# Kernel optimization log

Hardware: AMD Instinct MI355X
Metric: run time of the kernel (lower is better)

The kernel has to match this reference:

```python
import jax, jax.numpy as jnp
import numpy as np

WIN = (7, 7)
SHIFT = (3, 3)
HEADS = 8


def _rel_index():
    coords = np.stack(np.meshgrid(np.arange(WIN[0]), np.arange(WIN[1]), indexing='ij')).reshape(2, -1)
    rel = (coords[:, :, None] - coords[:, None, :]).transpose(1, 2, 0)  # [N,N,2]
    rel[:, :, 0] += WIN[0] - 1
    rel[:, :, 1] += WIN[1] - 1
    rel[:, :, 0] *= 2 * WIN[1] - 1
    return jnp.asarray(rel.sum(-1).reshape(-1).astype(np.int32))  # [N*N]


def _attn_mask(pad_H, pad_W):
    # standard Swin shifted-window mask (intended behavior of the source's mask block)
    img = np.zeros((pad_H, pad_W), np.float32)
    cnt = 0
    for h in ((0, -WIN[0]), (-WIN[0], -SHIFT[0]), (-SHIFT[0], None)):
        for w in ((0, -WIN[1]), (-WIN[1], -SHIFT[1]), (-SHIFT[1], None)):
            img[h[0]:h[1], w[0]:w[1]] = cnt
            cnt += 1
    nHw, nWw = pad_H // WIN[0], pad_W // WIN[1]
    m = img.reshape(nHw, WIN[0], nWw, WIN[1]).transpose(0, 2, 1, 3).reshape(nHw * nWw, WIN[0] * WIN[1])
    diff = m[:, None, :] - m[:, :, None]  # [nW, N, N]
    return jnp.asarray(np.where(diff != 0, -100.0, 0.0).astype(np.float32))


def setup_inputs() -> dict:
    key = jax.random.key(0)
    ks = jax.random.split(key, 6)
    B, H, W, C = 32, 56, 56, 256
    return {
        'x': jax.random.normal(ks[0], (B, H, W, C), jnp.float32),
        'qkv_weight': jax.random.normal(ks[1], (3 * C, C), jnp.float32) * (C ** -0.5),
        'qkv_bias': jnp.zeros((3 * C,), jnp.float32),
        'proj_weight': jax.random.normal(ks[2], (C, C), jnp.float32) * (C ** -0.5),
        'proj_bias': jnp.zeros((C,), jnp.float32),
        'rel_bias_table': jax.random.normal(ks[3], ((2 * WIN[0] - 1) * (2 * WIN[1] - 1), HEADS), jnp.float32) * 0.02,
        'rel_index': _rel_index(),
    }


def reference(x, qkv_weight, qkv_bias, proj_weight, proj_bias, rel_bias_table, rel_index):
    B, H, W, C = x.shape
    hd = C // HEADS
    N = WIN[0] * WIN[1]
    # relative position bias: [1, heads, N, N]
    bias = rel_bias_table[rel_index].reshape(N, N, HEADS).transpose(2, 0, 1)[None]
    # H, W chosen divisible by window -> pad is a no-op; cyclic shift
    xs = jnp.roll(x, (-SHIFT[0], -SHIFT[1]), axis=(1, 2))
    nHw, nWw = H // WIN[0], W // WIN[1]
    nW = nHw * nWw
    xw = xs.reshape(B, nHw, WIN[0], nWw, WIN[1], C).transpose(0, 1, 3, 2, 4, 5).reshape(B * nW, N, C)
    qkv = xw @ qkv_weight.T + qkv_bias                           # [B*nW, N, 3C]
    qkv = qkv.reshape(B * nW, N, 3, HEADS, hd).transpose(2, 0, 3, 1, 4)
    q, k, v = qkv[0] * hd ** -0.5, qkv[1], qkv[2]                # [B*nW, heads, N, hd]
    attn = jnp.einsum('whnd,whmd->whnm', q, k) + bias            # [B*nW, heads, N, N]
    mask = _attn_mask(H, W)                                      # [nW, N, N]
    attn = attn.reshape(B, nW, HEADS, N, N) + mask[None, :, None]
    attn = jax.nn.softmax(attn, axis=-1).reshape(B * nW, HEADS, N, N)
    out = jnp.einsum('whnm,whmd->wnhd', attn, v).reshape(B * nW, N, C)
    out = out @ proj_weight.T + proj_bias
    out = out.reshape(B, nHw, nWw, WIN[0], WIN[1], C).transpose(0, 1, 3, 2, 4, 5).reshape(B, H, W, C)
    out = jnp.roll(out, (SHIFT[0], SHIFT[1]), axis=(1, 2))
    return out
```

## Files before the change

kernel.cpp:

```cpp
#include <hip/hip_runtime.h>

typedef float f32x4 __attribute__((ext_vector_type(4)));
typedef __bf16 bf16x4 __attribute__((ext_vector_type(4)));
typedef __bf16 bf16x8 __attribute__((ext_vector_type(8)));
typedef short s16x4 __attribute__((ext_vector_type(4)));

#define DEVI static __device__ __forceinline__

DEVI f32x4 mfma_k32(bf16x8 a, bf16x8 b, f32x4 c) {
    return __builtin_amdgcn_mfma_f32_16x16x32_bf16(a, b, c, 0, 0, 0);
}

union B4 { bf16x4 h; s16x4 s; };
DEVI f32x4 mfma_k16(bf16x4 a, bf16x4 b, f32x4 c) {
    B4 ua, ub; ua.h = a; ub.h = b;
    return __builtin_amdgcn_mfma_f32_16x16x16bf16_1k(ua.s, ub.s, c, 0, 0, 0);
}

union F8 { bf16x8 v; bf16x4 h[2]; };

DEVI bf16x8 ld8_lds(const __bf16* p) {
    F8 f;
    f.h[0] = *(const bf16x4*)p;
    f.h[1] = *(const bf16x4*)(p + 4);
    return f.v;
}
DEVI bf16x8 ld8_gb(const __bf16* p) { return *(const bf16x8*)p; }
DEVI bf16x8 ldf8(const float* p) {
    f32x4 a = *(const f32x4*)p;
    f32x4 b = *(const f32x4*)(p + 4);
    F8 f;
#pragma unroll
    for (int j = 0; j < 4; ++j) {
        f.h[0][j] = (__bf16)a[j];
        f.h[1][j] = (__bf16)b[j];
    }
    return f.v;
}
DEVI bf16x4 pk4(f32x4 v) {
    bf16x4 r;
#pragma unroll
    for (int j = 0; j < 4; ++j) r[j] = (__bf16)v[j];
    return r;
}

__global__ __launch_bounds__(256) void k_pre(const float* __restrict__ wqkv,
                                             const float* __restrict__ wp,
                                             const float* __restrict__ btab,
                                             __bf16* __restrict__ wout,
                                             float* __restrict__ bmout) {
    int bid = blockIdx.x;
    if (bid < 128) {
        int i = bid * 256 + threadIdx.x;
        int t = i >> 9, kc = (i >> 6) & 7, l = i & 63;
        int row = t * 16 + (l & 15);
        int col = kc * 32 + (l >> 4) * 8;
        const float* src = (t < 48) ? (wqkv + row * 256 + col)
                                    : (wp + (row - 768) * 256 + col);
        f32x4 a = *(const f32x4*)src;
        f32x4 b = *(const f32x4*)(src + 4);
        F8 f;
#pragma unroll
        for (int j = 0; j < 4; ++j) { f.h[0][j] = (__bf16)a[j]; f.h[1][j] = (__bf16)b[j]; }
        *(bf16x8*)(wout + (size_t)i * 8) = f.v;
    } else {
        int i = (bid - 128) * 256 + threadIdx.x;
        int r = i & 3, lane = (i >> 2) & 63;
        int kt = (i >> 8) & 3, qt = (i >> 10) & 3, h = (i >> 12) & 7, cls = i >> 15;
        int li = lane & 15, g = lane >> 4;
        int q = 16 * qt + li;
        int key = 16 * kt + 4 * g + r;
        float v;
        if (key >= 49) {
            v = -30000.f;
        } else if (q >= 49) {
            v = 0.f;
        } else {
            int qi = q / 7, qj = q - 7 * qi;
            int ki = key / 7, kj = key - 7 * ki;
            float bias = btab[((qi - ki + 6) * 13 + (qj - kj + 6)) * 8 + h];
            int ch = cls >> 1, cw = cls & 1;
            int gq = (ch ? (qi < 4 ? 1 : 2) : 0) * 3 + (cw ? (qj < 4 ? 1 : 2) : 0);
            int gk = (ch ? (ki < 4 ? 1 : 2) : 0) * 3 + (cw ? (kj < 4 ? 1 : 2) : 0);
            v = bias + ((gq != gk) ? -100.f : 0.f);
        }
        bmout[i] = v;
    }
}

__global__ __launch_bounds__(512)
__attribute__((amdgpu_waves_per_eu(4))) void k_swin(
    const float* __restrict__ x,
    const __bf16* __restrict__ wb,
    const float* __restrict__ bqkv,
    const float* __restrict__ bm,
    const float* __restrict__ pbias,
    float* __restrict__ out)
{
    __shared__ __align__(16) unsigned char smem[51216];
    __bf16* xw = (__bf16*)(smem);
    __bf16* cb = (__bf16*)(smem + 25480);
    unsigned* obase = (unsigned*)(smem + 50960);

    const int tid = threadIdx.x;
    const int wid = tid >> 6, lane = tid & 63;
    const int li = lane & 15, g = lane >> 4;
    const int blk = blockIdx.x;
    const int b = blk >> 6, wi = blk & 63;
    const int wh = wi >> 3, ww = wi & 7;
    const int h = wid;
    const int cls = ((wh == 7) ? 2 : 0) + ((ww == 7) ? 1 : 0);

    for (int c = tid; c < 49 * 32; c += 512) {
        int tok = c >> 5, part = c & 31;
        int i = tok / 7, j = tok - 7 * i;
        int r = wh * 7 + i + 3;  if (r >= 56) r -= 56;
        int cc = ww * 7 + j + 3; if (cc >= 56) cc -= 56;
        F8 f; f.v = ldf8(x + (((size_t)(b * 56 + r) * 56 + cc) << 8) + (part << 3));
        __bf16* dst = xw + tok * 260 + (part << 3);
        *(bf16x4*)dst = f.h[0];
        *(bf16x4*)(dst + 4) = f.h[1];
    }
    if (tid < 49) {
        int i = tid / 7, j = tid - 7 * i;
        int r = wh * 7 + i + 3;  if (r >= 56) r -= 56;
        int cc = ww * 7 + j + 3; if (cc >= 56) cc -= 56;
        obase[tid] = ((unsigned)((b * 56 + r) * 56 + cc)) << 8;
    }
    __syncthreads();

    const f32x4 zf = {0.f, 0.f, 0.f, 0.f};
    const __bf16* wqb = wb + (size_t)(2 * h) * 4096 + lane * 8;
    const __bf16* wkb = wqb + 16 * 4096;
    const __bf16* wvb = wqb + 32 * 4096;

    bf16x4 qf[4][2], kf[4][2];
    {
        f32x4 qa[2][4], ka[2][4];
#pragma unroll
        for (int ct = 0; ct < 2; ++ct)
#pragma unroll
            for (int tt = 0; tt < 4; ++tt) { qa[ct][tt] = zf; ka[ct][tt] = zf; }

#pragma unroll
        for (int kc = 0; kc < 8; ++kc) {
            bf16x8 xf[4];
#pragma unroll
            for (int tt = 0; tt < 4; ++tt) {
                int row = 16 * tt + li; if (row > 48) row = 48;
                xf[tt] = ld8_lds(xw + row * 260 + kc * 32 + g * 8);
            }
#pragma unroll
            for (int ct = 0; ct < 2; ++ct) {
                bf16x8 aq = ld8_gb(wqb + ct * 4096 + kc * 512);
                bf16x8 ak = ld8_gb(wkb + ct * 4096 + kc * 512);
#pragma unroll
                for (int tt = 0; tt < 4; ++tt) {
                    qa[ct][tt] = mfma_k32(aq, xf[tt], qa[ct][tt]);
                    ka[ct][tt] = mfma_k32(ak, xf[tt], ka[ct][tt]);
                }
            }
        }
#pragma unroll
        for (int ct = 0; ct < 2; ++ct) {
            f32x4 bq = *(const f32x4*)(bqkv + h * 32 + 16 * ct + 4 * g);
            f32x4 bk = *(const f32x4*)(bqkv + 256 + h * 32 + 16 * ct + 4 * g);
#pragma unroll
            for (int tt = 0; tt < 4; ++tt)
#pragma unroll
                for (int r = 0; r < 4; ++r) {
                    qf[tt][ct][r] = (__bf16)((qa[ct][tt][r] + bq[r]) * 0.17677669529663687f);
                    kf[tt][ct][r] = (__bf16)(ka[ct][tt][r] + bk[r]);
                }
        }
    }
    __builtin_amdgcn_sched_barrier(0);

    bf16x4 vf[2][4];
    {
        f32x4 va[4][2];
#pragma unroll
        for (int tt = 0; tt < 4; ++tt)
#pragma unroll
            for (int ct = 0; ct < 2; ++ct) va[tt][ct] = zf;
#pragma unroll
        for (int kc = 0; kc < 8; ++kc) {
            bf16x8 bv0 = ld8_gb(wvb + kc * 512);
            bf16x8 bv1 = ld8_gb(wvb + 4096 + kc * 512);
#pragma unroll
            for (int tt = 0; tt < 4; ++tt) {
                int row = 16 * tt + li; if (row > 48) row = 48;
                bf16x8 xf = ld8_lds(xw + row * 260 + kc * 32 + g * 8);
                va[tt][0] = mfma_k32(xf, bv0, va[tt][0]);
                va[tt][1] = mfma_k32(xf, bv1, va[tt][1]);
            }
        }
#pragma unroll
        for (int ct = 0; ct < 2; ++ct) {
            float bv = bqkv[512 + h * 32 + 16 * ct + li];
#pragma unroll
            for (int tt = 0; tt < 4; ++tt)
#pragma unroll
                for (int r = 0; r < 4; ++r)
                    vf[ct][tt][r] = (__bf16)(va[tt][ct][r] + bv);
        }
    }
    __builtin_amdgcn_sched_barrier(0);

    const float* bmq = bm + cls * 32768 + h * 4096 + lane * 4;
    bf16x4 osv[4][2];
#pragma unroll
    for (int qt = 0; qt < 4; ++qt) {
        f32x4 sv[4];
#pragma unroll
        for (int kt = 0; kt < 4; ++kt) {
            f32x4 acc = *(const f32x4*)(bmq + qt * 1024 + kt * 256);
            acc = mfma_k16(kf[kt][0], qf[qt][0], acc);
            acc = mfma_k16(kf[kt][1], qf[qt][1], acc);
            sv[kt] = acc;
        }
        float mx = fmaxf(fmaxf(sv[0][0], sv[0][1]), fmaxf(sv[0][2], sv[0][3]));
#pragma unroll
        for (int kt = 1; kt < 4; ++kt)
#pragma unroll
            for (int r = 0; r < 4; ++r) mx = fmaxf(mx, sv[kt][r]);
        mx = fmaxf(mx, __shfl_xor(mx, 16));
        mx = fmaxf(mx, __shfl_xor(mx, 32));
        float sum = 0.f;
#pragma unroll
        for (int kt = 0; kt < 4; ++kt)
#pragma unroll
            for (int r = 0; r < 4; ++r) {
                float e = __expf(sv[kt][r] - mx);
                sv[kt][r] = e;
                sum += e;
            }
        sum += __shfl_xor(sum, 16);
        sum += __shfl_xor(sum, 32);
        float inv = 1.0f / sum;
        bf16x4 pp[4];
#pragma unroll
        for (int kt = 0; kt < 4; ++kt)
#pragma unroll
            for (int r = 0; r < 4; ++r) pp[kt][r] = (__bf16)(sv[kt][r] * inv);
#pragma unroll
        for (int dt = 0; dt < 2; ++dt) {
            f32x4 acc = zf;
#pragma unroll
            for (int kt = 0; kt < 4; ++kt)
                acc = mfma_k16(pp[kt], vf[dt][kt], acc);
            osv[qt][dt] = pk4(acc);
        }
    }

#pragma unroll
    for (int qt = 0; qt < 4; ++qt)
#pragma unroll
        for (int r = 0; r < 4; ++r) {
            int q = 16 * qt + 4 * g + r;
            if (q < 49) {
#pragma unroll
                for (int dt = 0; dt < 2; ++dt)
                    cb[q * 260 + 32 * h + 16 * dt + li] = osv[qt][dt][r];
            }
        }
    __syncthreads();

    const int pm = wid >> 2, pn = wid & 3;
    f32x4 pacc[2][4];
#pragma unroll
    for (int mt = 0; mt < 2; ++mt)
#pragma unroll
        for (int nt = 0; nt < 4; ++nt) pacc[mt][nt] = zf;

    const __bf16* wpb = wb + (size_t)(48 + 4 * pn) * 4096 + lane * 8;
#pragma unroll
    for (int kc = 0; kc < 8; ++kc) {
        bf16x8 a[2];
#pragma unroll
        for (int mt = 0; mt < 2; ++mt) {
            int row = 32 * pm + 16 * mt + li; if (row > 48) row = 48;
            a[mt] = ld8_lds(cb + row * 260 + kc * 32 + g * 8);
        }
#pragma unroll
        for (int nt = 0; nt < 4; ++nt) {
            bf16x8 bb = ld8_gb(wpb + nt * 4096 + kc * 512);
#pragma unroll
            for (int mt = 0; mt < 2; ++mt)
                pacc[mt][nt] = mfma_k32(a[mt], bb, pacc[mt][nt]);
        }
    }

#pragma unroll
    for (int nt = 0; nt < 4; ++nt) {
        int o = 64 * pn + 16 * nt + li;
        float bias = pbias[o];
#pragma unroll
        for (int mt = 0; mt < 2; ++mt)
#pragma unroll
            for (int r = 0; r < 4; ++r) {
                int n = 32 * pm + 16 * mt + 4 * g + r;
                if (n < 49)
                    out[obase[n] + (unsigned)o] = pacc[mt][nt][r] + bias;
            }
    }
}

extern "C" void kernel_launch(void* const* d_in, const int* in_sizes, int n_in,
                              void* d_out, int out_size, void* d_ws, size_t ws_size,
                              hipStream_t stream) {
    const float* x    = (const float*)d_in[0];
    const float* wqkv = (const float*)d_in[1];
    const float* bqkv = (const float*)d_in[2];
    const float* wp   = (const float*)d_in[3];
    const float* pb   = (const float*)d_in[4];
    const float* btab = (const float*)d_in[5];
    float* out = (float*)d_out;

    __bf16* wbuf = (__bf16*)d_ws;
    float* bm = (float*)((char*)d_ws + 524288);
    k_pre<<<640, 256, 0, stream>>>(wqkv, wp, btab, wbuf, bm);
    k_swin<<<2048, 512, 0, stream>>>(x, wbuf, bqkv, bm, pb, out);
}
```

Measured before the change: 275.7 us.

## Process four windows per block with double-buffered x staging and prefetch

Each block now handles four consecutive windows instead of one, and the grid shrinks from 2048 to 512 blocks. The x tile is double-buffered in LDS: the next window's fp32 input is loaded into registers during the attention phase and written as bf16 after it, so global load latency overlaps compute. The softmax also drops its row-max subtraction and adds the bias/mask after the MFMA rather than using it as the accumulator init. The trade-offs are more LDS per block (lower occupancy), a grid of exactly one wave, and exposure to exp overflow if logits are ever large.

```diff
diff --git a/kernel.cpp b/kernel.cpp
--- a/kernel.cpp
+++ b/kernel.cpp
@@ -26,22 +26,31 @@
     return f.v;
 }
 DEVI bf16x8 ld8_gb(const __bf16* p) { return *(const bf16x8*)p; }
-DEVI bf16x8 ldf8(const float* p) {
-    f32x4 a = *(const f32x4*)p;
-    f32x4 b = *(const f32x4*)(p + 4);
-    F8 f;
-#pragma unroll
-    for (int j = 0; j < 4; ++j) {
-        f.h[0][j] = (__bf16)a[j];
-        f.h[1][j] = (__bf16)b[j];
-    }
-    return f.v;
-}
 DEVI bf16x4 pk4(f32x4 v) {
     bf16x4 r;
 #pragma unroll
     for (int j = 0; j < 4; ++j) r[j] = (__bf16)v[j];
     return r;
+}
+
+DEVI size_t stage_src_off(int w, int t) {
+    int bb = w >> 6, wi = w & 63, wh = wi >> 3, ww = wi & 7;
+    int tok = t >> 3, p0 = (t & 7) * 4;
+    int i = tok / 7, j = tok - 7 * i;
+    int r = wh * 7 + i + 3;  if (r >= 56) r -= 56;
+    int cc = ww * 7 + j + 3; if (cc >= 56) cc -= 56;
+    return (((size_t)(bb * 56 + r) * 56 + cc) << 8) + (p0 << 3);
+}
+DEVI int stage_dst_off(int t) {
+    int tok = t >> 3, p0 = (t & 7) * 4;
+    return tok * 260 + p0 * 8;
+}
+DEVI unsigned out_base(int w, int tok) {
+    int bb = w >> 6, wi = w & 63, wh = wi >> 3, ww = wi & 7;
+    int i = tok / 7, j = tok - 7 * i;
+    int r = wh * 7 + i + 3;  if (r >= 56) r -= 56;
+    int cc = ww * 7 + j + 3; if (cc >= 56) cc -= 56;
+    return ((unsigned)((bb * 56 + r) * 56 + cc)) << 8;
 }
 
 __global__ __launch_bounds__(256) void k_pre(const float* __restrict__ wqkv,
@@ -97,212 +106,237 @@
     const float* __restrict__ pbias,
     float* __restrict__ out)
 {
-    __shared__ __align__(16) unsigned char smem[51216];
-    __bf16* xw = (__bf16*)(smem);
-    __bf16* cb = (__bf16*)(smem + 25480);
-    unsigned* obase = (unsigned*)(smem + 50960);
+    __shared__ __align__(16) unsigned char smem[76840];
+    __bf16* xw0 = (__bf16*)(smem);
+    __bf16* cb = (__bf16*)(smem + 50960);
+    unsigned* obase = (unsigned*)(smem + 76440);
 
     const int tid = threadIdx.x;
     const int wid = tid >> 6, lane = tid & 63;
     const int li = lane & 15, g = lane >> 4;
-    const int blk = blockIdx.x;
-    const int b = blk >> 6, wi = blk & 63;
-    const int wh = wi >> 3, ww = wi & 7;
     const int h = wid;
-    const int cls = ((wh == 7) ? 2 : 0) + ((ww == 7) ? 1 : 0);
-
-    for (int c = tid; c < 49 * 32; c += 512) {
-        int tok = c >> 5, part = c & 31;
-        int i = tok / 7, j = tok - 7 * i;
-        int r = wh * 7 + i + 3;  if (r >= 56) r -= 56;
-        int cc = ww * 7 + j + 3; if (cc >= 56) cc -= 56;
-        F8 f; f.v = ldf8(x + (((size_t)(b * 56 + r) * 56 + cc) << 8) + (part << 3));
-        __bf16* dst = xw + tok * 260 + (part << 3);
-        *(bf16x4*)dst = f.h[0];
-        *(bf16x4*)(dst + 4) = f.h[1];
-    }
-    if (tid < 49) {
-        int i = tid / 7, j = tid - 7 * i;
-        int r = wh * 7 + i + 3;  if (r >= 56) r -= 56;
-        int cc = ww * 7 + j + 3; if (cc >= 56) cc -= 56;
-        obase[tid] = ((unsigned)((b * 56 + r) * 56 + cc)) << 8;
-    }
-    __syncthreads();
-
+    const int pm = wid >> 2, pn = wid & 3;
     const f32x4 zf = {0.f, 0.f, 0.f, 0.f};
+
     const __bf16* wqb = wb + (size_t)(2 * h) * 4096 + lane * 8;
     const __bf16* wkb = wqb + 16 * 4096;
     const __bf16* wvb = wqb + 32 * 4096;
-
-    bf16x4 qf[4][2], kf[4][2];
-    {
-        f32x4 qa[2][4], ka[2][4];
-#pragma unroll
-        for (int ct = 0; ct < 2; ++ct)
-#pragma unroll
-            for (int tt = 0; tt < 4; ++tt) { qa[ct][tt] = zf; ka[ct][tt] = zf; }
+    const __bf16* wpb = wb + (size_t)(48 + 4 * pn) * 4096 + lane * 8;
+
+    const int w0 = blockIdx.x * 4;
+
+    if (tid < 392) {
+        f32x4 sa[4][2];
+        const float* p = x + stage_src_off(w0, tid);
+#pragma unroll
+        for (int s = 0; s < 4; ++s) {
+            sa[s][0] = *(const f32x4*)(p + s * 8);
+            sa[s][1] = *(const f32x4*)(p + s * 8 + 4);
+        }
+        __bf16* dst = xw0 + stage_dst_off(tid);
+#pragma unroll
+        for (int s = 0; s < 4; ++s) {
+            F8 f;
+#pragma unroll
+            for (int j = 0; j < 4; ++j) {
+                f.h[0][j] = (__bf16)sa[s][0][j];
+                f.h[1][j] = (__bf16)sa[s][1][j];
+            }
+            *(bf16x4*)(dst + s * 8) = f.h[0];
+            *(bf16x4*)(dst + s * 8 + 4) = f.h[1];
+        }
+    }
+    if (tid < 49) obase[tid] = out_base(w0, tid);
+    __syncthreads();
+
+    for (int it = 0; it < 4; ++it) {
+        const int w = w0 + it;
+        const int wi = w & 63;
+        const int cls = (((wi >> 3) == 7) ? 2 : 0) + (((wi & 7) == 7) ? 1 : 0);
+        const int cur = it & 1, nxt = cur ^ 1;
+        const __bf16* xwc = xw0 + cur * 12740;
+
+        bf16x4 qf[4][2], kf[4][2];
+        {
+            f32x4 qa[2][4], ka[2][4];
+#pragma unroll
+            for (int ct = 0; ct < 2; ++ct)
+#pragma unroll
+                for (int tt = 0; tt < 4; ++tt) { qa[ct][tt] = zf; ka[ct][tt] = zf; }
+
+#pragma unroll
+            for (int kc = 0; kc < 8; ++kc) {
+                bf16x8 xf[4];
+#pragma unroll
+                for (int tt = 0; tt < 4; ++tt) {
+                    int row = 16 * tt + li; if (row > 48) row = 48;
+                    xf[tt] = ld8_lds(xwc + row * 260 + kc * 32 + g * 8);
+                }
+#pragma unroll
+                for (int ct = 0; ct < 2; ++ct) {
+                    bf16x8 aq = ld8_gb(wqb + ct * 4096 + kc * 512);
+                    bf16x8 ak = ld8_gb(wkb + ct * 4096 + kc * 512);
+#pragma unroll
+                    for (int tt = 0; tt < 4; ++tt) {
+                        qa[ct][tt] = mfma_k32(aq, xf[tt], qa[ct][tt]);
+                        ka[ct][tt] = mfma_k32(ak, xf[tt], ka[ct][tt]);
+                    }
+                }
+            }
+#pragma unroll
+            for (int ct = 0; ct < 2; ++ct) {
+                f32x4 bq = *(const f32x4*)(bqkv + h * 32 + 16 * ct + 4 * g);
+                f32x4 bk = *(const f32x4*)(bqkv + 256 + h * 32 + 16 * ct + 4 * g);
+#pragma unroll
+                for (int tt = 0; tt < 4; ++tt)
+#pragma unroll
+                    for (int r = 0; r < 4; ++r) {
+                        qf[tt][ct][r] = (__bf16)((qa[ct][tt][r] + bq[r]) * 0.17677669529663687f);
+                        kf[tt][ct][r] = (__bf16)(ka[ct][tt][r] + bk[r]);
+                    }
+            }
+        }
+        __builtin_amdgcn_sched_barrier(0);
+
+        bf16x4 vf[2][4];
+        {
+            f32x4 va[4][2];
+#pragma unroll
+            for (int tt = 0; tt < 4; ++tt)
+#pragma unroll
+                for (int ct = 0; ct < 2; ++ct) va[tt][ct] = zf;
+#pragma unroll
+            for (int kc = 0; kc < 8; ++kc) {
+                bf16x8 bv0 = ld8_gb(wvb + kc * 512);
+                bf16x8 bv1 = ld8_gb(wvb + 4096 + kc * 512);
+#pragma unroll
+                for (int tt = 0; tt < 4; ++tt) {
+                    int row = 16 * tt + li; if (row > 48) row = 48;
+                    bf16x8 xf = ld8_lds(xwc + row * 260 + kc * 32 + g * 8);
+                    va[tt][0] = mfma_k32(xf, bv0, va[tt][0]);
+                    va[tt][1] = mfma_k32(xf, bv1, va[tt][1]);
+                }
+            }
+#pragma unroll
+            for (int ct = 0; ct < 2; ++ct) {
+                float bv = bqkv[512 + h * 32 + 16 * ct + li];
+#pragma unroll
+                for (int tt = 0; tt < 4; ++tt)
+#pragma unroll
+                    for (int r = 0; r < 4; ++r)
+                        vf[ct][tt][r] = (__bf16)(va[tt][ct][r] + bv);
+            }
+        }
+        __builtin_amdgcn_sched_barrier(0);
+
+        const bool hn = (it < 3);
+        f32x4 sa[4][2];
+        if (hn && tid < 392) {
+            const float* p = x + stage_src_off(w + 1, tid);
+#pragma unroll
+            for (int s = 0; s < 4; ++s) {
+                sa[s][0] = *(const f32x4*)(p + s * 8);
+                sa[s][1] = *(const f32x4*)(p + s * 8 + 4);
+            }
+        }
+
+        const float* bmq = bm + cls * 32768 + h * 4096 + lane * 4;
+#pragma unroll
+        for (int qt = 0; qt < 4; ++qt) {
+            f32x4 sv[4];
+#pragma unroll
+            for (int kt = 0; kt < 4; ++kt) {
+                f32x4 acc = zf;
+                acc = mfma_k16(kf[kt][0], qf[qt][0], acc);
+                acc = mfma_k16(kf[kt][1], qf[qt][1], acc);
+                sv[kt] = acc + *(const f32x4*)(bmq + qt * 1024 + kt * 256);
+            }
+            float sum = 0.f;
+#pragma unroll
+            for (int kt = 0; kt < 4; ++kt)
+#pragma unroll
+                for (int r = 0; r < 4; ++r) {
+                    float e = __expf(sv[kt][r]);
+                    sv[kt][r] = e;
+                    sum += e;
+                }
+            sum += __shfl_xor(sum, 16);
+            sum += __shfl_xor(sum, 32);
+            float inv = 1.0f / sum;
+            bf16x4 pp[4];
+#pragma unroll
+            for (int kt = 0; kt < 4; ++kt)
+#pragma unroll
+                for (int r = 0; r < 4; ++r) pp[kt][r] = (__bf16)(sv[kt][r] * inv);
+#pragma unroll
+            for (int dt = 0; dt < 2; ++dt) {
+                f32x4 acc = zf;
+#pragma unroll
+                for (int kt = 0; kt < 4; ++kt)
+                    acc = mfma_k16(pp[kt], vf[dt][kt], acc);
+                bf16x4 o4 = pk4(acc);
+#pragma unroll
+                for (int r = 0; r < 4; ++r) {
+                    int q = 16 * qt + 4 * g + r;
+                    if (q < 49) cb[q * 260 + 32 * h + 16 * dt + li] = o4[r];
+                }
+            }
+        }
+
+        if (hn && tid < 392) {
+            __bf16* dst = xw0 + nxt * 12740 + stage_dst_off(tid);
+#pragma unroll
+            for (int s = 0; s < 4; ++s) {
+                F8 f;
+#pragma unroll
+                for (int j = 0; j < 4; ++j) {
+                    f.h[0][j] = (__bf16)sa[s][0][j];
+                    f.h[1][j] = (__bf16)sa[s][1][j];
+                }
+                *(bf16x4*)(dst + s * 8) = f.h[0];
+                *(bf16x4*)(dst + s * 8 + 4) = f.h[1];
+            }
+        }
+        if (hn && tid < 49) obase[nxt * 49 + tid] = out_base(w + 1, tid);
+        __syncthreads();
+
+        f32x4 pacc[2][4];
+#pragma unroll
+        for (int mt = 0; mt < 2; ++mt)
+#pragma unroll
+            for (int nt = 0; nt < 4; ++nt) pacc[mt][nt] = zf;
 
 #pragma unroll
         for (int kc = 0; kc < 8; ++kc) {
-            bf16x8 xf[4];
-#pragma unroll
-            for (int tt = 0; tt < 4; ++tt) {
-                int row = 16 * tt + li; if (row > 48) row = 48;
-                xf[tt] = ld8_lds(xw + row * 260 + kc * 32 + g * 8);
-            }
-#pragma unroll
-            for (int ct = 0; ct < 2; ++ct) {
-                bf16x8 aq = ld8_gb(wqb + ct * 4096 + kc * 512);
-                bf16x8 ak = ld8_gb(wkb + ct * 4096 + kc * 512);
-#pragma unroll
-                for (int tt = 0; tt < 4; ++tt) {
-                    qa[ct][tt] = mfma_k32(aq, xf[tt], qa[ct][tt]);
-                    ka[ct][tt] = mfma_k32(ak, xf[tt], ka[ct][tt]);
-                }
-            }
-        }
-#pragma unroll
-        for (int ct = 0; ct < 2; ++ct) {
-            f32x4 bq = *(const f32x4*)(bqkv + h * 32 + 16 * ct + 4 * g);
-            f32x4 bk = *(const f32x4*)(bqkv + 256 + h * 32 + 16 * ct + 4 * g);
-#pragma unroll
-            for (int tt = 0; tt < 4; ++tt)
+            bf16x8 a[2];
+#pragma unroll
+            for (int mt = 0; mt < 2; ++mt) {
+                int row = 32 * pm + 16 * mt + li; if (row > 48) row = 48;
+                a[mt] = ld8_lds(cb + row * 260 + kc * 32 + g * 8);
+            }
+#pragma unroll
+            for (int nt = 0; nt < 4; ++nt) {
+                bf16x8 bb = ld8_gb(wpb + nt * 4096 + kc * 512);
+#pragma unroll
+                for (int mt = 0; mt < 2; ++mt)
+                    pacc[mt][nt] = mfma_k32(a[mt], bb, pacc[mt][nt]);
+            }
+        }
+
+#pragma unroll
+        for (int nt = 0; nt < 4; ++nt) {
+            int o = 64 * pn + 16 * nt + li;
+            float bias = pbias[o];
+#pragma unroll
+            for (int mt = 0; mt < 2; ++mt)
 #pragma unroll
                 for (int r = 0; r < 4; ++r) {
-                    qf[tt][ct][r] = (__bf16)((qa[ct][tt][r] + bq[r]) * 0.17677669529663687f);
-                    kf[tt][ct][r] = (__bf16)(ka[ct][tt][r] + bk[r]);
-                }
-        }
-    }
-    __builtin_amdgcn_sched_barrier(0);
-
-    bf16x4 vf[2][4];
-    {
-        f32x4 va[4][2];
-#pragma unroll
-        for (int tt = 0; tt < 4; ++tt)
-#pragma unroll
-            for (int ct = 0; ct < 2; ++ct) va[tt][ct] = zf;
-#pragma unroll
-        for (int kc = 0; kc < 8; ++kc) {
-            bf16x8 bv0 = ld8_gb(wvb + kc * 512);
-            bf16x8 bv1 = ld8_gb(wvb + 4096 + kc * 512);
-#pragma unroll
-            for (int tt = 0; tt < 4; ++tt) {
-                int row = 16 * tt + li; if (row > 48) row = 48;
-                bf16x8 xf = ld8_lds(xw + row * 260 + kc * 32 + g * 8);
-                va[tt][0] = mfma_k32(xf, bv0, va[tt][0]);
-                va[tt][1] = mfma_k32(xf, bv1, va[tt][1]);
-            }
-        }
-#pragma unroll
-        for (int ct = 0; ct < 2; ++ct) {
-            float bv = bqkv[512 + h * 32 + 16 * ct + li];
-#pragma unroll
-            for (int tt = 0; tt < 4; ++tt)
-#pragma unroll
-                for (int r = 0; r < 4; ++r)
-                    vf[ct][tt][r] = (__bf16)(va[tt][ct][r] + bv);
-        }
-    }
-    __builtin_amdgcn_sched_barrier(0);
-
-    const float* bmq = bm + cls * 32768 + h * 4096 + lane * 4;
-    bf16x4 osv[4][2];
-#pragma unroll
-    for (int qt = 0; qt < 4; ++qt) {
-        f32x4 sv[4];
-#pragma unroll
-        for (int kt = 0; kt < 4; ++kt) {
-            f32x4 acc = *(const f32x4*)(bmq + qt * 1024 + kt * 256);
-            acc = mfma_k16(kf[kt][0], qf[qt][0], acc);
-            acc = mfma_k16(kf[kt][1], qf[qt][1], acc);
-            sv[kt] = acc;
-        }
-        float mx = fmaxf(fmaxf(sv[0][0], sv[0][1]), fmaxf(sv[0][2], sv[0][3]));
-#pragma unroll
-        for (int kt = 1; kt < 4; ++kt)
-#pragma unroll
-            for (int r = 0; r < 4; ++r) mx = fmaxf(mx, sv[kt][r]);
-        mx = fmaxf(mx, __shfl_xor(mx, 16));
-        mx = fmaxf(mx, __shfl_xor(mx, 32));
-        float sum = 0.f;
-#pragma unroll
-        for (int kt = 0; kt < 4; ++kt)
-#pragma unroll
-            for (int r = 0; r < 4; ++r) {
-                float e = __expf(sv[kt][r] - mx);
-                sv[kt][r] = e;
-                sum += e;
-            }
-        sum += __shfl_xor(sum, 16);
-        sum += __shfl_xor(sum, 32);
-        float inv = 1.0f / sum;
-        bf16x4 pp[4];
-#pragma unroll
-        for (int kt = 0; kt < 4; ++kt)
-#pragma unroll
-            for (int r = 0; r < 4; ++r) pp[kt][r] = (__bf16)(sv[kt][r] * inv);
-#pragma unroll
-        for (int dt = 0; dt < 2; ++dt) {
-            f32x4 acc = zf;
-#pragma unroll
-            for (int kt = 0; kt < 4; ++kt)
-                acc = mfma_k16(pp[kt], vf[dt][kt], acc);
-            osv[qt][dt] = pk4(acc);
-        }
-    }
-
-#pragma unroll
-    for (int qt = 0; qt < 4; ++qt)
-#pragma unroll
-        for (int r = 0; r < 4; ++r) {
-            int q = 16 * qt + 4 * g + r;
-            if (q < 49) {
-#pragma unroll
-                for (int dt = 0; dt < 2; ++dt)
-                    cb[q * 260 + 32 * h + 16 * dt + li] = osv[qt][dt][r];
-            }
-        }
-    __syncthreads();
-
-    const int pm = wid >> 2, pn = wid & 3;
-    f32x4 pacc[2][4];
-#pragma unroll
-    for (int mt = 0; mt < 2; ++mt)
-#pragma unroll
-        for (int nt = 0; nt < 4; ++nt) pacc[mt][nt] = zf;
-
-    const __bf16* wpb = wb + (size_t)(48 + 4 * pn) * 4096 + lane * 8;
-#pragma unroll
-    for (int kc = 0; kc < 8; ++kc) {
-        bf16x8 a[2];
-#pragma unroll
-        for (int mt = 0; mt < 2; ++mt) {
-            int row = 32 * pm + 16 * mt + li; if (row > 48) row = 48;
-            a[mt] = ld8_lds(cb + row * 260 + kc * 32 + g * 8);
-        }
-#pragma unroll
-        for (int nt = 0; nt < 4; ++nt) {
-            bf16x8 bb = ld8_gb(wpb + nt * 4096 + kc * 512);
-#pragma unroll
-            for (int mt = 0; mt < 2; ++mt)
-                pacc[mt][nt] = mfma_k32(a[mt], bb, pacc[mt][nt]);
-        }
-    }
-
-#pragma unroll
-    for (int nt = 0; nt < 4; ++nt) {
-        int o = 64 * pn + 16 * nt + li;
-        float bias = pbias[o];
-#pragma unroll
-        for (int mt = 0; mt < 2; ++mt)
-#pragma unroll
-            for (int r = 0; r < 4; ++r) {
-                int n = 32 * pm + 16 * mt + 4 * g + r;
-                if (n < 49)
-                    out[obase[n] + (unsigned)o] = pacc[mt][nt][r] + bias;
-            }
+                    int n = 32 * pm + 16 * mt + 4 * g + r;
+                    if (n < 49)
+                        out[obase[cur * 49 + n] + (unsigned)o] = pacc[mt][nt][r] + bias;
+                }
+        }
+        __syncthreads();
     }
 }
 
@@ -320,5 +354,5 @@
     __bf16* wbuf = (__bf16*)d_ws;
     float* bm = (float*)((char*)d_ws + 524288);
     k_pre<<<640, 256, 0, stream>>>(wqkv, wp, btab, wbuf, bm);
-    k_swin<<<2048, 512, 0, stream>>>(x, wbuf, bqkv, bm, pb, out);
-}
+    k_swin<<<512, 512, 0, stream>>>(x, wbuf, bqkv, bm, pb, out);
+}
```

Measured after the change: 691.6 us. +150.8%, slower.

## Fold softmax scaling into weights, drop max pass, vectorize attention and output stores

Applied to the files above, without the earlier changes.

The Q scale and log2(e) are folded into the packed Q weights, and log2(e) into the bias/mask table. The per-row max reduction is removed, and the softmax now uses a hardware exp2 and rcp, with normalization applied after the PV product. QKV and projection biases now initialise the MFMA accumulators instead of being added afterwards. The PV and projection MFMA operands are swapped so each lane holds contiguous channels, which gives bf16x4 LDS stores and f32x4 global output stores in place of scalar ones. Skipping the max subtraction risks overflow if the logits become large.

```diff
diff --git a/kernel.cpp b/kernel.cpp
--- a/kernel.cpp
+++ b/kernel.cpp
@@ -7,6 +7,9 @@
 
 #define DEVI static __device__ __forceinline__
 
+#define LOG2E 1.4426950408889634f
+#define QSCALE (0.17677669529663687f * 1.4426950408889634f)
+
 DEVI f32x4 mfma_k32(bf16x8 a, bf16x8 b, f32x4 c) {
     return __builtin_amdgcn_mfma_f32_16x16x32_bf16(a, b, c, 0, 0, 0);
 }
@@ -16,6 +19,9 @@
     B4 ua, ub; ua.h = a; ub.h = b;
     return __builtin_amdgcn_mfma_f32_16x16x16bf16_1k(ua.s, ub.s, c, 0, 0, 0);
 }
+
+DEVI float exp2_hw(float x) { return __builtin_amdgcn_exp2f(x); }
+DEVI float rcp_hw(float x)  { return __builtin_amdgcn_rcpf(x); }
 
 union F8 { bf16x8 v; bf16x4 h[2]; };
 
@@ -57,11 +63,15 @@
         int col = kc * 32 + (l >> 4) * 8;
         const float* src = (t < 48) ? (wqkv + row * 256 + col)
                                     : (wp + (row - 768) * 256 + col);
+        float s = (t < 16) ? QSCALE : 1.0f;
         f32x4 a = *(const f32x4*)src;
         f32x4 b = *(const f32x4*)(src + 4);
         F8 f;
 #pragma unroll
-        for (int j = 0; j < 4; ++j) { f.h[0][j] = (__bf16)a[j]; f.h[1][j] = (__bf16)b[j]; }
+        for (int j = 0; j < 4; ++j) {
+            f.h[0][j] = (__bf16)(a[j] * s);
+            f.h[1][j] = (__bf16)(b[j] * s);
+        }
         *(bf16x8*)(wout + (size_t)i * 8) = f.v;
     } else {
         int i = (bid - 128) * 256 + threadIdx.x;
@@ -84,7 +94,7 @@
             int gk = (ch ? (ki < 4 ? 1 : 2) : 0) * 3 + (cw ? (kj < 4 ? 1 : 2) : 0);
             v = bias + ((gq != gk) ? -100.f : 0.f);
         }
-        bmout[i] = v;
+        bmout[i] = v * LOG2E;
     }
 }
 
@@ -136,11 +146,17 @@
 
     bf16x4 qf[4][2], kf[4][2];
     {
+        f32x4 bq[2], bk[2];
+#pragma unroll
+        for (int ct = 0; ct < 2; ++ct) {
+            bq[ct] = *(const f32x4*)(bqkv + h * 32 + 16 * ct + 4 * g) * QSCALE;
+            bk[ct] = *(const f32x4*)(bqkv + 256 + h * 32 + 16 * ct + 4 * g);
+        }
         f32x4 qa[2][4], ka[2][4];
 #pragma unroll
         for (int ct = 0; ct < 2; ++ct)
 #pragma unroll
-            for (int tt = 0; tt < 4; ++tt) { qa[ct][tt] = zf; ka[ct][tt] = zf; }
+            for (int tt = 0; tt < 4; ++tt) { qa[ct][tt] = bq[ct]; ka[ct][tt] = bk[ct]; }
 
 #pragma unroll
         for (int kc = 0; kc < 8; ++kc) {
@@ -162,53 +178,50 @@
             }
         }
 #pragma unroll
-        for (int ct = 0; ct < 2; ++ct) {
-            f32x4 bq = *(const f32x4*)(bqkv + h * 32 + 16 * ct + 4 * g);
-            f32x4 bk = *(const f32x4*)(bqkv + 256 + h * 32 + 16 * ct + 4 * g);
+        for (int ct = 0; ct < 2; ++ct)
 #pragma unroll
             for (int tt = 0; tt < 4; ++tt)
 #pragma unroll
                 for (int r = 0; r < 4; ++r) {
-                    qf[tt][ct][r] = (__bf16)((qa[ct][tt][r] + bq[r]) * 0.17677669529663687f);
-                    kf[tt][ct][r] = (__bf16)(ka[ct][tt][r] + bk[r]);
+                    qf[tt][ct][r] = (__bf16)qa[ct][tt][r];
+                    kf[tt][ct][r] = (__bf16)ka[ct][tt][r];
                 }
-        }
     }
     __builtin_amdgcn_sched_barrier(0);
 
     bf16x4 vf[2][4];
     {
+        float bv0 = bqkv[512 + h * 32 + li];
+        float bv1 = bqkv[512 + h * 32 + 16 + li];
         f32x4 va[4][2];
 #pragma unroll
-        for (int tt = 0; tt < 4; ++tt)
-#pragma unroll
-            for (int ct = 0; ct < 2; ++ct) va[tt][ct] = zf;
+        for (int tt = 0; tt < 4; ++tt) {
+            va[tt][0] = (f32x4){bv0, bv0, bv0, bv0};
+            va[tt][1] = (f32x4){bv1, bv1, bv1, bv1};
+        }
 #pragma unroll
         for (int kc = 0; kc < 8; ++kc) {
-            bf16x8 bv0 = ld8_gb(wvb + kc * 512);
-            bf16x8 bv1 = ld8_gb(wvb + 4096 + kc * 512);
+            bf16x8 bvw0 = ld8_gb(wvb + kc * 512);
+            bf16x8 bvw1 = ld8_gb(wvb + 4096 + kc * 512);
 #pragma unroll
             for (int tt = 0; tt < 4; ++tt) {
                 int row = 16 * tt + li; if (row > 48) row = 48;
                 bf16x8 xf = ld8_lds(xw + row * 260 + kc * 32 + g * 8);
-                va[tt][0] = mfma_k32(xf, bv0, va[tt][0]);
-                va[tt][1] = mfma_k32(xf, bv1, va[tt][1]);
+                va[tt][0] = mfma_k32(xf, bvw0, va[tt][0]);
+                va[tt][1] = mfma_k32(xf, bvw1, va[tt][1]);
             }
         }
 #pragma unroll
-        for (int ct = 0; ct < 2; ++ct) {
-            float bv = bqkv[512 + h * 32 + 16 * ct + li];
+        for (int ct = 0; ct < 2; ++ct)
 #pragma unroll
             for (int tt = 0; tt < 4; ++tt)
 #pragma unroll
                 for (int r = 0; r < 4; ++r)
-                    vf[ct][tt][r] = (__bf16)(va[tt][ct][r] + bv);
-        }
+                    vf[ct][tt][r] = (__bf16)va[tt][ct][r];
     }
     __builtin_amdgcn_sched_barrier(0);
 
     const float* bmq = bm + cls * 32768 + h * 4096 + lane * 4;
-    bf16x4 osv[4][2];
 #pragma unroll
     for (int qt = 0; qt < 4; ++qt) {
         f32x4 sv[4];
@@ -219,61 +232,51 @@
             acc = mfma_k16(kf[kt][1], qf[qt][1], acc);
             sv[kt] = acc;
         }
-        float mx = fmaxf(fmaxf(sv[0][0], sv[0][1]), fmaxf(sv[0][2], sv[0][3]));
-#pragma unroll
-        for (int kt = 1; kt < 4; ++kt)
-#pragma unroll
-            for (int r = 0; r < 4; ++r) mx = fmaxf(mx, sv[kt][r]);
-        mx = fmaxf(mx, __shfl_xor(mx, 16));
-        mx = fmaxf(mx, __shfl_xor(mx, 32));
         float sum = 0.f;
 #pragma unroll
         for (int kt = 0; kt < 4; ++kt)
 #pragma unroll
             for (int r = 0; r < 4; ++r) {
-                float e = __expf(sv[kt][r] - mx);
+                float e = exp2_hw(sv[kt][r]);
                 sv[kt][r] = e;
                 sum += e;
             }
         sum += __shfl_xor(sum, 16);
         sum += __shfl_xor(sum, 32);
-        float inv = 1.0f / sum;
+        float inv = rcp_hw(sum);
         bf16x4 pp[4];
 #pragma unroll
         for (int kt = 0; kt < 4; ++kt)
 #pragma unroll
-            for (int r = 0; r < 4; ++r) pp[kt][r] = (__bf16)(sv[kt][r] * inv);
+            for (int r = 0; r < 4; ++r) pp[kt][r] = (__bf16)sv[kt][r];
+        const int q = 16 * qt + li;
 #pragma unroll
         for (int dt = 0; dt < 2; ++dt) {
             f32x4 acc = zf;
 #pragma unroll
             for (int kt = 0; kt < 4; ++kt)
-                acc = mfma_k16(pp[kt], vf[dt][kt], acc);
-            osv[qt][dt] = pk4(acc);
-        }
-    }
-
-#pragma unroll
-    for (int qt = 0; qt < 4; ++qt)
-#pragma unroll
-        for (int r = 0; r < 4; ++r) {
-            int q = 16 * qt + 4 * g + r;
-            if (q < 49) {
-#pragma unroll
-                for (int dt = 0; dt < 2; ++dt)
-                    cb[q * 260 + 32 * h + 16 * dt + li] = osv[qt][dt][r];
-            }
-        }
+                acc = mfma_k16(vf[dt][kt], pp[kt], acc);
+            acc *= inv;
+            bf16x4 o4 = pk4(acc);
+            if (q < 49)
+                *(bf16x4*)(cb + q * 260 + 32 * h + 16 * dt + 4 * g) = o4;
+        }
+    }
     __syncthreads();
 
     const int pm = wid >> 2, pn = wid & 3;
+    const __bf16* wpb = wb + (size_t)(48 + 4 * pn) * 4096 + lane * 8;
+
+    f32x4 pb4[4];
+#pragma unroll
+    for (int nt = 0; nt < 4; ++nt)
+        pb4[nt] = *(const f32x4*)(pbias + 64 * pn + 16 * nt + 4 * g);
     f32x4 pacc[2][4];
 #pragma unroll
     for (int mt = 0; mt < 2; ++mt)
 #pragma unroll
-        for (int nt = 0; nt < 4; ++nt) pacc[mt][nt] = zf;
-
-    const __bf16* wpb = wb + (size_t)(48 + 4 * pn) * 4096 + lane * 8;
+        for (int nt = 0; nt < 4; ++nt) pacc[mt][nt] = pb4[nt];
+
 #pragma unroll
     for (int kc = 0; kc < 8; ++kc) {
         bf16x8 a[2];
@@ -287,22 +290,19 @@
             bf16x8 bb = ld8_gb(wpb + nt * 4096 + kc * 512);
 #pragma unroll
             for (int mt = 0; mt < 2; ++mt)
-                pacc[mt][nt] = mfma_k32(a[mt], bb, pacc[mt][nt]);
-        }
-    }
-
-#pragma unroll
-    for (int nt = 0; nt < 4; ++nt) {
-        int o = 64 * pn + 16 * nt + li;
-        float bias = pbias[o];
-#pragma unroll
-        for (int mt = 0; mt < 2; ++mt)
-#pragma unroll
-            for (int r = 0; r < 4; ++r) {
-                int n = 32 * pm + 16 * mt + 4 * g + r;
-                if (n < 49)
-                    out[obase[n] + (unsigned)o] = pacc[mt][nt][r] + bias;
-            }
+                pacc[mt][nt] = mfma_k32(bb, a[mt], pacc[mt][nt]);
+        }
+    }
+
+#pragma unroll
+    for (int mt = 0; mt < 2; ++mt) {
+        int tok = 32 * pm + 16 * mt + li;
+        if (tok < 49) {
+            float* op = out + obase[tok] + 64 * pn + 4 * g;
+#pragma unroll
+            for (int nt = 0; nt < 4; ++nt)
+                *(f32x4*)(op + 16 * nt) = pacc[mt][nt];
+        }
     }
 }
 
```

After: 269.4 us. 1.02x faster.
